# Kernel tuning notes

Measured on AMD Instinct MI355X. Metric: run time of the kernel, lower is better.

Reference implementation:

```python
import jax, jax.numpy as jnp
import numpy as np

EPS = 1e-5

def layer_norm(x, w, b):
    mu = jnp.mean(x, axis=-1, keepdims=True)
    var = jnp.var(x, axis=-1, keepdims=True)
    return (x - mu) * jax.lax.rsqrt(var + EPS) * w + b

def setup_inputs() -> dict:
    key = jax.random.key(0)
    ks = jax.random.split(key, 9)
    B, N, d, hidden = 1, 512, 64, 128
    s = 0.02
    return {
        "z": jax.random.normal(ks[0], (B, N, N, d), dtype=jnp.float32),
        "ln_in_w": jnp.ones((d,), jnp.float32),
        "ln_in_b": jnp.zeros((d,), jnp.float32),
        "Wp": jax.random.normal(ks[1], (d, 2 * hidden), jnp.float32) * s,
        "Wg": jax.random.normal(ks[2], (d, 2 * hidden), jnp.float32) * s,
        "ln_out_w": jnp.ones((hidden,), jnp.float32),
        "ln_out_b": jnp.zeros((hidden,), jnp.float32),
        "Wout": jax.random.normal(ks[3], (hidden, d), jnp.float32) * s,
        "Wgate": jax.random.normal(ks[4], (d, d), jnp.float32) * s,
    }

def reference(z, ln_in_w, ln_in_b, Wp, Wg, ln_out_w, ln_out_b, Wout, Wgate):
    # z: [B, N, N, d]
    h = layer_norm(z, ln_in_w, ln_in_b)
    p = h @ Wp                               # [B,N,N,2*hidden]
    g_in = jax.nn.sigmoid(h @ Wg)            # [B,N,N,2*hidden]
    pg = p * g_in
    a, b = jnp.split(pg, 2, axis=-1)         # each [B,N,N,hidden]
    # direction == 'outgoing'
    out = jnp.einsum('bikd,bjkd->bijd', a, b)  # [B,N,N,hidden]
    out = layer_norm(out, ln_out_w, ln_out_b)
    g_out = jax.nn.sigmoid(h @ Wgate)        # [B,N,N,d]
    return (out @ Wout) * g_out              # [B,N,N,d]
```

## Files before the change

### kernel.cpp

```cpp
#include <hip/hip_runtime.h>
#include <hip/hip_fp16.h>


typedef _Float16 half_t;
typedef _Float16 f16x4 __attribute__((ext_vector_type(4)));
typedef _Float16 f16x8 __attribute__((ext_vector_type(8)));
typedef float f32x4 __attribute__((ext_vector_type(4)));

#define NSEQ 512
#define HID 128
#define ROWS (NSEQ * NSEQ)

#define GLOAD16(src, dst)                                                        \
    __builtin_amdgcn_global_load_lds(                                            \
        (const __attribute__((address_space(1))) void*)(src),                    \
        (__attribute__((address_space(3))) void*)(dst), 16, 0, 0)

__device__ __forceinline__ float fast_sigmoid(float x) {
    float e = __builtin_amdgcn_exp2f(-1.44269504088896f * x);
    return __builtin_amdgcn_rcpf(1.f + e);
}

__global__ void k_prep_w(const float* __restrict__ Wp, const float* __restrict__ Wg,
                         const float* __restrict__ Wgate,
                         const float* __restrict__ ln_out_w, const float* __restrict__ ln_out_b,
                         const float* __restrict__ Wout,
                         half_t* __restrict__ Wimg, half_t* __restrict__ W1t,
                         float* __restrict__ s1, float* __restrict__ s2) {
    int bid = blockIdx.x, t = threadIdx.x;
    if (bid < 18) {
        int chunk = bid * 256 + t;
        int ch = chunk >= 2304;
        int q = chunk - ch * 2304;
        int lr = q >> 3, slot = q & 7;
        int co = slot ^ (lr & 7);
        int grow;
        if (lr < 128)      grow = ch * 128 + lr;
        else if (lr < 256) grow = 256 + ch * 128 + (lr - 128);
        else               grow = 512 + ch * 32 + (lr - 256);
        f16x8 vals;
        #pragma unroll
        for (int j = 0; j < 8; ++j) {
            int l = co * 8 + j;
            float v;
            if (grow < 256)      v = Wp[l * 256 + grow];
            else if (grow < 512) v = Wg[l * 256 + (grow - 256)];
            else                 v = Wgate[l * 64 + (grow - 512)];
            vals[j] = (half_t)v;
        }
        *(f16x8*)(Wimg + (size_t)chunk * 8) = vals;
    } else {
        #pragma unroll
        for (int i = 0; i < 32; ++i) {
            int idx = t * 32 + i;
            int o = idx >> 7, c = idx & 127;
            W1t[idx] = (half_t)(ln_out_w[c] * Wout[c * 64 + o]);
        }
        if (t < 64) {
            float a1 = 0.f, a2 = 0.f;
            for (int c = 0; c < 128; ++c) {
                float wo = Wout[c * 64 + t];
                a1 += ln_out_w[c] * wo;
                a2 += ln_out_b[c] * wo;
            }
            s1[t] = a1; s2[t] = a2;
        }
    }
}

__global__ __launch_bounds__(256) void k_ln_in(const float* __restrict__ z,
                                               const float* __restrict__ w,
                                               const float* __restrict__ b,
                                               half_t* __restrict__ h) {
    int t = threadIdx.x;
    int row = blockIdx.x * 16 + (t >> 4);
    int c4 = t & 15;
    f32x4 x = *(const f32x4*)(z + (size_t)row * 64 + c4 * 4);
    float s = x[0] + x[1] + x[2] + x[3];
    float s2 = x[0]*x[0] + x[1]*x[1] + x[2]*x[2] + x[3]*x[3];
    #pragma unroll
    for (int off = 1; off < 16; off <<= 1) {
        s  += __shfl_xor(s,  off, 64);
        s2 += __shfl_xor(s2, off, 64);
    }
    float mu = s * (1.f / 64.f);
    float var = s2 * (1.f / 64.f) - mu * mu;
    float rs = rsqrtf(var + 1e-5f);
    f32x4 wv = *(const f32x4*)(w + c4 * 4);
    f32x4 bv = *(const f32x4*)(b + c4 * 4);
    f16x4 o;
    #pragma unroll
    for (int j = 0; j < 4; ++j)
        o[j] = (half_t)((x[j] - mu) * rs * wv[j] + bv[j]);
    *(f16x4*)(h + (size_t)row * 64 + c4 * 4) = o;
}

__global__ __launch_bounds__(256) void k_proj(const half_t* __restrict__ h,
                                              const half_t* __restrict__ Wimg,
                                              half_t* __restrict__ a_t,
                                              half_t* __restrict__ b_t,
                                              half_t* __restrict__ g_out) {
    __shared__ half_t Wl[288 * 64];
    __shared__ half_t pgl[64 * 66];

    int t = threadIdx.x;
    int ch = blockIdx.y;
    int bx = blockIdx.x;
    int r0 = bx * 128;
    int wid = t >> 6, lane = t & 63;
    int m = lane & 15, g = lane >> 4;

    const half_t* wsrc = Wimg + (size_t)ch * 2304 * 8;
    #pragma unroll
    for (int it = 0; it < 9; ++it) {
        int cb = it * 256 + wid * 64;
        GLOAD16(wsrc + (size_t)(cb + lane) * 8, Wl + (size_t)cb * 8);
    }

    f16x8 af[2][2];
    #pragma unroll
    for (int rp = 0; rp < 2; ++rp)
        #pragma unroll
        for (int ks = 0; ks < 2; ++ks)
            af[rp][ks] = *(const f16x8*)(h + (size_t)(r0 + rp * 64 + wid * 16 + m) * 64
                                           + ks * 32 + g * 8);

    __syncthreads();

    half_t* dst = (ch == 0) ? a_t : b_t;
    int swz = (bx >> 3) & 3;

    #pragma unroll
    for (int rp = 0; rp < 2; ++rp) {
        int rbase = r0 + rp * 64;
        for (int grp = 0; grp < 2; ++grp) {
            #pragma unroll
            for (int pt4 = 0; pt4 < 4; ++pt4) {
                int pt = grp * 4 + pt4;
                f32x4 accp = {0.f, 0.f, 0.f, 0.f}, accg = {0.f, 0.f, 0.f, 0.f};
                #pragma unroll
                for (int ks = 0; ks < 2; ++ks) {
                    int kb = (ks * 32 + g * 8) * 2;
                    int lrp = pt * 16 + m;
                    f16x8 bp = *(const f16x8*)((char*)Wl + lrp * 128 + (kb ^ ((lrp & 7) << 4)));
                    int lrg = 128 + pt * 16 + m;
                    f16x8 bg = *(const f16x8*)((char*)Wl + lrg * 128 + (kb ^ ((lrg & 7) << 4)));
                    accp = __builtin_amdgcn_mfma_f32_16x16x32_f16(af[rp][ks], bp, accp, 0, 0, 0);
                    accg = __builtin_amdgcn_mfma_f32_16x16x32_f16(af[rp][ks], bg, accg, 0, 0, 0);
                }
                f16x4 pk;
                #pragma unroll
                for (int r = 0; r < 4; ++r)
                    pk[r] = (half_t)(accp[r] * fast_sigmoid(accg[r]));
                *(f16x4*)&pgl[(pt4 * 16 + m) * 66 + wid * 16 + g * 4] = pk;
            }
            __syncthreads();
            #pragma unroll
            for (int it = 0; it < 2; ++it) {
                int chunk = it * 256 + t;
                int cl = chunk >> 3, r8 = chunk & 7;
                f16x8 v = *(const f16x8*)&pgl[cl * 66 + r8 * 8];
                int dk = (r8 & 4) | ((r8 & 3) ^ swz);
                *(f16x8*)(dst + (size_t)(grp * 64 + cl) * ROWS + rbase + dk * 8) = v;
            }
            __syncthreads();
        }

        #pragma unroll
        for (int gt = 0; gt < 2; ++gt) {
            f32x4 acc = {0.f, 0.f, 0.f, 0.f};
            #pragma unroll
            for (int ks = 0; ks < 2; ++ks) {
                int kb = (ks * 32 + g * 8) * 2;
                int lr = 256 + gt * 16 + m;
                f16x8 bb = *(const f16x8*)((char*)Wl + lr * 128 + (kb ^ ((lr & 7) << 4)));
                acc = __builtin_amdgcn_mfma_f32_16x16x32_f16(af[rp][ks], bb, acc, 0, 0, 0);
            }
            int och = ch * 32 + gt * 16 + m;
            #pragma unroll
            for (int r = 0; r < 4; ++r) {
                float og = fast_sigmoid(acc[r]);
                int grow = rbase + wid * 16 + g * 4 + r;
                g_out[(size_t)grow * 64 + och] = (half_t)og;
            }
        }
    }
}

#define EBUF 8192
__global__ __launch_bounds__(256) void k_einsum(const half_t* __restrict__ a_t,
                                                const half_t* __restrict__ b_t,
                                                half_t* __restrict__ out_mid) {
    __shared__ half_t lds[3 * EBUF];

    int t = threadIdx.x;
    int wid = t >> 6, lane = t & 63;
    int m = lane & 15, g = lane >> 4;

    int bid = blockIdx.x;
    int xcd = bid & 7;
    int rest = bid >> 3;
    int gen = rest >> 6;
    int local = rest & 63;
    int c = xcd + 8 * (gen * 4 + (local >> 4));
    int tile = local & 15;
    int i0 = (tile >> 2) * 128, j0 = (tile & 3) * 128;

    const half_t* A = a_t + (size_t)c * ROWS;
    const half_t* B = b_t + (size_t)c * ROWS;
    int wr = wid >> 1, wc = wid & 1;

    f32x4 acc[4][4] = {};

#define STAGE_A(ktt, base, it)                                                    \
    {                                                                             \
        int cb = (it) * 256 + wid * 64;              \
        int chunk = cb + lane;                                                    \
        GLOAD16(A + (size_t)(i0 + (chunk >> 2)) * 512 + (ktt) * 32 + (chunk & 3) * 8, \
                (base) + (size_t)cb * 8);                                         \
    }
#define STAGE_B(ktt, base, it)                                                    \
    {                                                                             \
        int cb = (it) * 256 + wid * 64;                                           \
        int chunk = cb + lane;                                                    \
        GLOAD16(B + (size_t)(j0 + (chunk >> 2)) * 512 + (ktt) * 32 + (chunk & 3) * 8, \
                (base) + 4096 + (size_t)cb * 8);                                  \
    }
#define STAGE_ALL(ktt, base)                                                      \
    STAGE_A(ktt, base, 0) STAGE_A(ktt, base, 1) STAGE_B(ktt, base, 0) STAGE_B(ktt, base, 1)

    STAGE_ALL(0, lds)
    STAGE_ALL(1, lds + EBUF)

    #pragma unroll
    for (int kt = 0; kt < 16; ++kt) {
        const half_t* Ac = lds + (kt % 3) * EBUF;
        const half_t* Bc = Ac + 4096;
        half_t* nxt = lds + ((kt + 2) % 3) * EBUF;

        if (kt <= 14) asm volatile("s_waitcnt vmcnt(4)" ::: "memory");
        else          asm volatile("s_waitcnt vmcnt(0)" ::: "memory");
        __builtin_amdgcn_s_barrier();
        __builtin_amdgcn_sched_barrier(0);

        f16x8 bf[4];
        #pragma unroll
        for (int ni = 0; ni < 4; ++ni) {
            int lrow = wc * 64 + ni * 16 + m;
            bf[ni] = *(const f16x8*)((const char*)Bc + lrow * 64 +
                                     ((g ^ ((lrow >> 1) & 3)) << 4));
        }
        #pragma unroll
        for (int mi = 0; mi < 4; ++mi) {
            int lrow = wr * 64 + mi * 16 + m;
            f16x8 afr = *(const f16x8*)((const char*)Ac + lrow * 64 +
                                        ((g ^ ((lrow >> 1) & 3)) << 4));
            if (kt < 14) {
                if (mi == 0)      STAGE_A(kt + 2, nxt, 0)
                else if (mi == 1) STAGE_A(kt + 2, nxt, 1)
                else if (mi == 2) STAGE_B(kt + 2, nxt, 0)
                else              STAGE_B(kt + 2, nxt, 1)
            }
            __builtin_amdgcn_s_setprio(1);
            #pragma unroll
            for (int ni = 0; ni < 4; ++ni)
                acc[mi][ni] = __builtin_amdgcn_mfma_f32_16x16x32_f16(afr, bf[ni], acc[mi][ni], 0, 0, 0);
            __builtin_amdgcn_s_setprio(0);
        }
    }
#undef STAGE_ALL
#undef STAGE_B
#undef STAGE_A

    half_t* O = out_mid + (size_t)c * ROWS;
    #pragma unroll
    for (int mi = 0; mi < 4; ++mi) {
        #pragma unroll
        for (int ni = 0; ni < 4; ++ni) {
            int row = i0 + wr * 64 + mi * 16 + g * 4;
            int col = j0 + wc * 64 + ni * 16 + m;
            #pragma unroll
            for (int r2 = 0; r2 < 4; ++r2)
                O[(size_t)(row + r2) * 512 + col] = (half_t)acc[mi][ni][r2];
        }
    }
}

__global__ __launch_bounds__(256) void k_final(const half_t* __restrict__ out_mid,
                                               const half_t* __restrict__ W1t,
                                               const float* __restrict__ s1g,
                                               const float* __restrict__ s2g,
                                               const half_t* __restrict__ g_out,
                                               float* __restrict__ out) {
    __shared__ half_t midl[128 * 64];
    __shared__ half_t midt[64 * 128];
    __shared__ half_t w1l[64 * 128];
    __shared__ half_t gl[64 * 72];
    __shared__ float smu[64], srs[64], s1l[64], s2l[64];

    int t = threadIdx.x;
    int pos0 = blockIdx.x * 64;

    #pragma unroll
    for (int it = 0; it < 4; ++it) {
        int chunk = it * 256 + t;
        int cc = chunk >> 3, co = chunk & 7;
        *(uint4*)((char*)midl + cc * 128 + co * 16) =
            *(const uint4*)(out_mid + (size_t)cc * ROWS + pos0 + co * 8);
    }
    #pragma unroll
    for (int it = 0; it < 4; ++it) {
        int chunk = it * 256 + t;
        int row = chunk >> 4, slot = chunk & 15;
        *(uint4*)((char*)w1l + row * 256 + ((slot * 16) ^ ((row & 7) << 4))) =
            *(const uint4*)(W1t + row * 128 + slot * 8);
    }
    #pragma unroll
    for (int it = 0; it < 2; ++it) {
        int chunk = it * 256 + t;
        int row = chunk >> 3, co = chunk & 7;
        *(uint4*)((char*)gl + row * 144 + co * 16) =
            *(const uint4*)(g_out + (size_t)(pos0 + row) * 64 + co * 8);
    }
    if (t < 64) { s1l[t] = s1g[t]; s2l[t] = s2g[t]; }
    __syncthreads();

    {
        int p = t >> 2, q = t & 3;
        float s = 0.f, s2 = 0.f;
        #pragma unroll
        for (int cc4 = 0; cc4 < 4; ++cc4) {
            f16x8 pack;
            #pragma unroll
            for (int j = 0; j < 8; ++j) {
                half_t hv = midl[(q * 32 + cc4 * 8 + j) * 64 + p];
                float v = (float)hv;
                s += v; s2 += v * v;
                pack[j] = hv;
            }
            int slot = q * 4 + cc4;
            *(f16x8*)((char*)midt + p * 256 + ((slot * 16) ^ ((p & 7) << 4))) = pack;
        }
        s  += __shfl_xor(s, 1, 64);  s  += __shfl_xor(s, 2, 64);
        s2 += __shfl_xor(s2, 1, 64); s2 += __shfl_xor(s2, 2, 64);
        if (q == 0) {
            float mu = s * (1.f / 128.f);
            float var = s2 * (1.f / 128.f) - mu * mu;
            smu[p] = mu;
            srs[p] = rsqrtf(var + 1e-5f);
        }
    }
    __syncthreads();

    int wid = t >> 6, lane = t & 63;
    int m = lane & 15, g = lane >> 4;

    f32x4 acc[4] = {};
    #pragma unroll
    for (int ks = 0; ks < 4; ++ks) {
        int arow = wid * 16 + m;
        f16x8 af = *(const f16x8*)((char*)midt + arow * 256 +
                                   (((4 * ks + g) * 16) ^ ((arow & 7) << 4)));
        #pragma unroll
        for (int ni = 0; ni < 4; ++ni) {
            int brow = ni * 16 + m;
            f16x8 bf = *(const f16x8*)((char*)w1l + brow * 256 +
                                       (((4 * ks + g) * 16) ^ ((brow & 7) << 4)));
            acc[ni] = __builtin_amdgcn_mfma_f32_16x16x32_f16(af, bf, acc[ni], 0, 0, 0);
        }
    }

    #pragma unroll
    for (int ni = 0; ni < 4; ++ni) {
        int o = ni * 16 + m;
        float v1 = s1l[o], v2 = s2l[o];
        #pragma unroll
        for (int r = 0; r < 4; ++r) {
            int lrow = wid * 16 + g * 4 + r;
            float mu = smu[lrow], rs = srs[lrow];
            float val = acc[ni][r] * rs - mu * rs * v1 + v2;
            float gate = (float)gl[lrow * 72 + o];
            out[(size_t)(pos0 + lrow) * 64 + o] = val * gate;
        }
    }
}

extern "C" void kernel_launch(void* const* d_in, const int* in_sizes, int n_in,
                              void* d_out, int out_size, void* d_ws, size_t ws_size,
                              hipStream_t stream) {
    const float* z        = (const float*)d_in[0];
    const float* ln_in_w  = (const float*)d_in[1];
    const float* ln_in_b  = (const float*)d_in[2];
    const float* Wp       = (const float*)d_in[3];
    const float* Wg       = (const float*)d_in[4];
    const float* ln_out_w = (const float*)d_in[5];
    const float* ln_out_b = (const float*)d_in[6];
    const float* Wout     = (const float*)d_in[7];
    const float* Wgate    = (const float*)d_in[8];
    float* out = (float*)d_out;

    char* wsb = (char*)d_ws;
    half_t* Wimg = (half_t*)wsb;
    half_t* W1t  = (half_t*)(wsb + 81920);
    float*  s1   = (float*)(wsb + 98304);
    float*  s2   = (float*)(wsb + 98560);
    half_t* a_t  = (half_t*)(wsb + 131072);
    half_t* b_t  = a_t + (size_t)HID * ROWS;
    half_t* gout = b_t + (size_t)HID * ROWS;
    half_t* omid = gout + (size_t)ROWS * 64;
    half_t* h    = omid;

    k_prep_w<<<dim3(19), dim3(256), 0, stream>>>(Wp, Wg, Wgate, ln_out_w, ln_out_b, Wout,
                                                 Wimg, W1t, s1, s2);
    k_ln_in<<<dim3(ROWS / 16), dim3(256), 0, stream>>>(z, ln_in_w, ln_in_b, h);
    k_proj<<<dim3(ROWS / 128, 2), dim3(256), 0, stream>>>(h, Wimg, a_t, b_t, gout);
    k_einsum<<<dim3(2048), dim3(256), 0, stream>>>(a_t, b_t, omid);
    k_final<<<dim3(ROWS / 64), dim3(256), 0, stream>>>(omid, W1t, s1, s2, gout, out);
}
```

Measured before the change: 158.4 us.

## Write projection outputs directly from MFMA registers, drop LDS transpose staging

```diff
diff --git a/kernel.cpp b/kernel.cpp
--- a/kernel.cpp
+++ b/kernel.cpp
@@ -101,12 +101,11 @@
                                               half_t* __restrict__ b_t,
                                               half_t* __restrict__ g_out) {
     __shared__ half_t Wl[288 * 64];
-    __shared__ half_t pgl[64 * 66];
 
     int t = threadIdx.x;
     int ch = blockIdx.y;
     int bx = blockIdx.x;
-    int r0 = bx * 128;
+    int r0 = bx * 64;
     int wid = t >> 6, lane = t & 63;
     int m = lane & 15, g = lane >> 4;
 
@@ -117,72 +116,56 @@
         GLOAD16(wsrc + (size_t)(cb + lane) * 8, Wl + (size_t)cb * 8);
     }
 
-    f16x8 af[2][2];
-    #pragma unroll
-    for (int rp = 0; rp < 2; ++rp)
-        #pragma unroll
-        for (int ks = 0; ks < 2; ++ks)
-            af[rp][ks] = *(const f16x8*)(h + (size_t)(r0 + rp * 64 + wid * 16 + m) * 64
-                                           + ks * 32 + g * 8);
+    int growbase = r0 + wid * 16;
+    f16x8 af[2];
+    #pragma unroll
+    for (int ks = 0; ks < 2; ++ks)
+        af[ks] = *(const f16x8*)(h + (size_t)(growbase + m) * 64 + ks * 32 + g * 8);
 
     __syncthreads();
 
     half_t* dst = (ch == 0) ? a_t : b_t;
-    int swz = (bx >> 3) & 3;
-
-    #pragma unroll
-    for (int rp = 0; rp < 2; ++rp) {
-        int rbase = r0 + rp * 64;
-        for (int grp = 0; grp < 2; ++grp) {
-            #pragma unroll
-            for (int pt4 = 0; pt4 < 4; ++pt4) {
-                int pt = grp * 4 + pt4;
-                f32x4 accp = {0.f, 0.f, 0.f, 0.f}, accg = {0.f, 0.f, 0.f, 0.f};
-                #pragma unroll
-                for (int ks = 0; ks < 2; ++ks) {
-                    int kb = (ks * 32 + g * 8) * 2;
-                    int lrp = pt * 16 + m;
-                    f16x8 bp = *(const f16x8*)((char*)Wl + lrp * 128 + (kb ^ ((lrp & 7) << 4)));
-                    int lrg = 128 + pt * 16 + m;
-                    f16x8 bg = *(const f16x8*)((char*)Wl + lrg * 128 + (kb ^ ((lrg & 7) << 4)));
-                    accp = __builtin_amdgcn_mfma_f32_16x16x32_f16(af[rp][ks], bp, accp, 0, 0, 0);
-                    accg = __builtin_amdgcn_mfma_f32_16x16x32_f16(af[rp][ks], bg, accg, 0, 0, 0);
-                }
-                f16x4 pk;
-                #pragma unroll
-                for (int r = 0; r < 4; ++r)
-                    pk[r] = (half_t)(accp[r] * fast_sigmoid(accg[r]));
-                *(f16x4*)&pgl[(pt4 * 16 + m) * 66 + wid * 16 + g * 4] = pk;
-            }
-            __syncthreads();
-            #pragma unroll
-            for (int it = 0; it < 2; ++it) {
-                int chunk = it * 256 + t;
-                int cl = chunk >> 3, r8 = chunk & 7;
-                f16x8 v = *(const f16x8*)&pgl[cl * 66 + r8 * 8];
-                int dk = (r8 & 4) | ((r8 & 3) ^ swz);
-                *(f16x8*)(dst + (size_t)(grp * 64 + cl) * ROWS + rbase + dk * 8) = v;
-            }
-            __syncthreads();
-        }
-
-        #pragma unroll
-        for (int gt = 0; gt < 2; ++gt) {
-            f32x4 acc = {0.f, 0.f, 0.f, 0.f};
-            #pragma unroll
-            for (int ks = 0; ks < 2; ++ks) {
-                int kb = (ks * 32 + g * 8) * 2;
-                int lr = 256 + gt * 16 + m;
-                f16x8 bb = *(const f16x8*)((char*)Wl + lr * 128 + (kb ^ ((lr & 7) << 4)));
-                acc = __builtin_amdgcn_mfma_f32_16x16x32_f16(af[rp][ks], bb, acc, 0, 0, 0);
-            }
-            int och = ch * 32 + gt * 16 + m;
-            #pragma unroll
-            for (int r = 0; r < 4; ++r) {
-                float og = fast_sigmoid(acc[r]);
-                int grow = rbase + wid * 16 + g * 4 + r;
-                g_out[(size_t)grow * 64 + och] = (half_t)og;
-            }
+    int swz = (bx >> 4) & 3;
+    int r8 = wid * 2 + (g >> 1);
+    int dk = (r8 & 4) | ((r8 & 3) ^ swz);
+    size_t rowoff = (size_t)r0 + dk * 8 + (g & 1) * 4;
+
+    #pragma unroll
+    for (int pt = 0; pt < 8; ++pt) {
+        f32x4 accp = {0.f, 0.f, 0.f, 0.f}, accg = {0.f, 0.f, 0.f, 0.f};
+        #pragma unroll
+        for (int ks = 0; ks < 2; ++ks) {
+            int kb = (ks * 32 + g * 8) * 2;
+            int lrp = pt * 16 + m;
+            f16x8 bp = *(const f16x8*)((char*)Wl + lrp * 128 + (kb ^ ((lrp & 7) << 4)));
+            int lrg = 128 + pt * 16 + m;
+            f16x8 bg = *(const f16x8*)((char*)Wl + lrg * 128 + (kb ^ ((lrg & 7) << 4)));
+            accp = __builtin_amdgcn_mfma_f32_16x16x32_f16(af[ks], bp, accp, 0, 0, 0);
+            accg = __builtin_amdgcn_mfma_f32_16x16x32_f16(af[ks], bg, accg, 0, 0, 0);
+        }
+        f16x4 pk;
+        #pragma unroll
+        for (int r = 0; r < 4; ++r)
+            pk[r] = (half_t)(accp[r] * fast_sigmoid(accg[r]));
+        *(f16x4*)(dst + (size_t)(pt * 16 + m) * ROWS + rowoff) = pk;
+    }
+
+    #pragma unroll
+    for (int gt = 0; gt < 2; ++gt) {
+        f32x4 acc = {0.f, 0.f, 0.f, 0.f};
+        #pragma unroll
+        for (int ks = 0; ks < 2; ++ks) {
+            int kb = (ks * 32 + g * 8) * 2;
+            int lr = 256 + gt * 16 + m;
+            f16x8 bb = *(const f16x8*)((char*)Wl + lr * 128 + (kb ^ ((lr & 7) << 4)));
+            acc = __builtin_amdgcn_mfma_f32_16x16x32_f16(af[ks], bb, acc, 0, 0, 0);
+        }
+        int och = ch * 32 + gt * 16 + m;
+        #pragma unroll
+        for (int r = 0; r < 4; ++r) {
+            float og = fast_sigmoid(acc[r]);
+            int grow = growbase + g * 4 + r;
+            g_out[(size_t)grow * 64 + och] = (half_t)og;
         }
     }
 }
@@ -413,7 +396,7 @@
     k_prep_w<<<dim3(19), dim3(256), 0, stream>>>(Wp, Wg, Wgate, ln_out_w, ln_out_b, Wout,
                                                  Wimg, W1t, s1, s2);
     k_ln_in<<<dim3(ROWS / 16), dim3(256), 0, stream>>>(z, ln_in_w, ln_in_b, h);
-    k_proj<<<dim3(ROWS / 128, 2), dim3(256), 0, stream>>>(h, Wimg, a_t, b_t, gout);
+    k_proj<<<dim3(ROWS / 64, 2), dim3(256), 0, stream>>>(h, Wimg, a_t, b_t, gout);
     k_einsum<<<dim3(2048), dim3(256), 0, stream>>>(a_t, b_t, omid);
     k_final<<<dim3(ROWS / 64), dim3(256), 0, stream>>>(omid, W1t, s1, s2, gout, out);
 }
```

Result: slower. 172.5 us (+8.9%).
